# Performance work log

Hardware: AMD Instinct MI355X
Metric: run time of the kernel (lower is better)

## Reference

```python
import jax, jax.numpy as jnp
import numpy as np

BN_EPS = 1e-5


def setup_inputs() -> dict:
    key = jax.random.key(0)
    ks = jax.random.split(key, 12)
    N, F, H, E, ED, G, EMB = 59392, 116, 256, 950272, 5, 8, 16
    return {
        "x": jax.random.normal(ks[0], (N, F), dtype=jnp.float32),
        "edge_index": jax.random.randint(ks[1], (2, E), 0, N, dtype=jnp.int64),
        "edge_attr": jax.random.normal(ks[2], (E, ED), dtype=jnp.float32),
        "group_ids": jax.random.randint(ks[3], (N,), 0, G, dtype=jnp.int64),
        "group_emb": jax.random.normal(ks[4], (G, EMB), dtype=jnp.float32),
        "W_in": jax.random.normal(ks[5], (F + EMB, H), dtype=jnp.float32) * 0.05,
        "b_in": jnp.zeros((H,), dtype=jnp.float32),
        "gamma": jnp.ones((H,), dtype=jnp.float32),
        "beta": jnp.zeros((H,), dtype=jnp.float32),
        "We": jax.random.normal(ks[6], (ED, H), dtype=jnp.float32) * 0.05,
        "be": jnp.zeros((H,), dtype=jnp.float32),
        "W1": jax.random.normal(ks[7], (H, H), dtype=jnp.float32) * 0.05,
        "b1": jnp.zeros((H,), dtype=jnp.float32),
        "W2": jax.random.normal(ks[8], (H, H), dtype=jnp.float32) * 0.05,
        "b2": jnp.zeros((H,), dtype=jnp.float32),
    }


def reference(x, edge_index, edge_attr, group_ids, group_emb, W_in, b_in,
              gamma, beta, We, be, W1, b1, W2, b2):
    N = x.shape[0]
    # group-embedding concat (dropout is identity in eval mode)
    h = jnp.concatenate([x, group_emb[group_ids]], axis=-1)      # [N, F+EMB]
    # dynamically-created Linear + ReLU
    h = jax.nn.relu(h @ W_in + b_in)                              # [N, H]
    # BatchNorm over nodes (training stats, biased var)
    mu = jnp.mean(h, axis=0)
    var = jnp.mean(jnp.square(h - mu), axis=0)
    h = (h - mu) * jax.lax.rsqrt(var + BN_EPS) * gamma + beta
    # GINEConv: msg = ReLU(x_j + lin(edge_attr)); sum-aggregate at target
    src, dst = edge_index[0], edge_index[1]
    msg = jax.nn.relu(h[src] + edge_attr @ We + be)               # [E, H]
    agg = jax.ops.segment_sum(msg, dst, num_segments=N)          # [N, H]
    z = h + agg                                                   # (1+eps)*h, eps=0
    out = jax.nn.relu(z @ W1 + b1) @ W2 + b2                      # 2-layer MLP
    out = jax.nn.relu(out)
    return (out, edge_attr)
```

## Files before the change

kernel.cpp:

```cpp
#include <hip/hip_runtime.h>
#include <hip/hip_bf16.h>
#include <cstdint>
#include <cstddef>

#define H 256
#define EMB 16
#define ED 5
#define BN_EPS 1e-5f

typedef __attribute__((ext_vector_type(8))) short short8;
typedef __attribute__((ext_vector_type(4))) float f32x4;
typedef _Float16 h2 __attribute__((ext_vector_type(2)));

__device__ __forceinline__ unsigned short f2bf(float f) {
  unsigned int u = __float_as_uint(f);
  unsigned int r = (u + 0x7fffu + ((u >> 16) & 1u)) >> 16;
  return (unsigned short)r;
}
__device__ __forceinline__ unsigned int pk2bf(float a, float b) {
  return (unsigned int)f2bf(a) | ((unsigned int)f2bf(b) << 16);
}
__device__ __forceinline__ float bfhi(unsigned int u) {
  return __uint_as_float(u & 0xffff0000u);
}
__device__ __forceinline__ float bflo(unsigned int u) {
  return __uint_as_float(u << 16);
}
__device__ __forceinline__ h2 u2h2(unsigned int u) {
  union { unsigned int u; h2 h; } c;
  c.u = u;
  return c.h;
}
__device__ __forceinline__ unsigned int h22u(h2 h) {
  union { h2 h; unsigned int u; } c;
  c.h = h;
  return c.u;
}
__device__ __forceinline__ h2 mkh2(float a, float b) {
  h2 r;
  r.x = (_Float16)a;
  r.y = (_Float16)b;
  return r;
}

__global__ __launch_bounds__(256) void prep_kernel(
    const float* __restrict__ Win, const float* __restrict__ W1,
    const float* __restrict__ W2, const float* __restrict__ gemb,
    const float* __restrict__ b_in, unsigned short* __restrict__ Wtx,
    unsigned short* __restrict__ Wt1, unsigned short* __restrict__ Wt2,
    float* __restrict__ T, float* __restrict__ stats, int* __restrict__ deg,
    int N, int F, int G) {
  int idx = blockIdx.x * 256 + threadIdx.x;
  if (idx < 1024) stats[idx] = 0.f;
  if (idx < N) deg[idx] = 0;
  if (idx < 256 * 128) {
    int n = idx >> 7, k = idx & 127;
    Wtx[idx] = f2bf((k < F) ? Win[(size_t)k * H + n] : 0.f);
  } else if (idx < 256 * 128 + 65536) {
    int i2 = idx - 256 * 128;
    int n = i2 >> 8, k = i2 & 255;
    Wt1[i2] = f2bf(W1[(size_t)k * H + n]);
  } else if (idx < 256 * 128 + 131072) {
    int i2 = idx - 256 * 128 - 65536;
    int n = i2 >> 8, k = i2 & 255;
    Wt2[i2] = f2bf(W2[(size_t)k * H + n]);
  } else if (idx < 256 * 128 + 131072 + G * 256) {
    int i2 = idx - 256 * 128 - 131072;
    int g = i2 >> 8, c = i2 & 255;
    float s = b_in[c];
    #pragma unroll
    for (int k = 0; k < EMB; ++k)
      s = fmaf(gemb[g * EMB + k], Win[(size_t)(F + k) * H + c], s);
    T[i2] = s;
  }
}

__global__ __launch_bounds__(256) void gemm_in_kernel(
    const float* __restrict__ x, const int* __restrict__ gid,
    const unsigned short* __restrict__ Wtx, const float* __restrict__ T,
    unsigned short* __restrict__ h0, float* __restrict__ stats, int F) {
  const int m0 = blockIdx.y * 128;
  const int n0 = blockIdx.x * 128;
  const int tid = threadIdx.x;
  const int lane = tid & 63;
  const int wave = tid >> 6;
  const int wm = (wave & 1) * 64;
  const int wn = (wave >> 1) * 64;
  const int l16 = lane & 15;
  const int quad = lane >> 4;
  __shared__ __align__(16) unsigned short As[128][40];
  __shared__ __align__(16) unsigned short Bs[128][40];
  __shared__ float cs[128], css[128];
  if (tid < 128) {
    cs[tid] = 0.f;
    css[tid] = 0.f;
  }
  f32x4 acc[4][4] = {};
  const int srow = tid >> 1;
  const int half = tid & 1;
  for (int k0 = 0; k0 < 128; k0 += 32) {
    __syncthreads();
    {
      const float* xp = x + (size_t)(m0 + srow) * F;
      float4 xv[4];
      #pragma unroll
      for (int f = 0; f < 4; ++f) {
        int c = k0 + half * 16 + f * 4;
        xv[f] = (c < F) ? *(const float4*)(xp + c)
                        : make_float4(0.f, 0.f, 0.f, 0.f);
      }
      uint4 p0, p1;
      p0.x = pk2bf(xv[0].x, xv[0].y); p0.y = pk2bf(xv[0].z, xv[0].w);
      p0.z = pk2bf(xv[1].x, xv[1].y); p0.w = pk2bf(xv[1].z, xv[1].w);
      p1.x = pk2bf(xv[2].x, xv[2].y); p1.y = pk2bf(xv[2].z, xv[2].w);
      p1.z = pk2bf(xv[3].x, xv[3].y); p1.w = pk2bf(xv[3].z, xv[3].w);
      *(uint4*)(&As[srow][half * 16]) = p0;
      *(uint4*)(&As[srow][half * 16 + 8]) = p1;
    }
    {
      const unsigned short* wp = Wtx + (size_t)(n0 + srow) * 128 + k0 + half * 16;
      *(uint4*)(&Bs[srow][half * 16]) = *(const uint4*)wp;
      *(uint4*)(&Bs[srow][half * 16 + 8]) = *(const uint4*)(wp + 8);
    }
    __syncthreads();
    short8 af[4], bf[4];
    #pragma unroll
    for (int i = 0; i < 4; ++i)
      af[i] = *(const short8*)(&As[wm + i * 16 + l16][quad * 8]);
    #pragma unroll
    for (int j = 0; j < 4; ++j)
      bf[j] = *(const short8*)(&Bs[wn + j * 16 + l16][quad * 8]);
    #pragma unroll
    for (int i = 0; i < 4; ++i)
      #pragma unroll
      for (int j = 0; j < 4; ++j)
        acc[i][j] = __builtin_amdgcn_mfma_f32_16x16x32_bf16(af[i], bf[j],
                                                            acc[i][j], 0, 0, 0);
  }
  int gi[4][4];
  #pragma unroll
  for (int i = 0; i < 4; ++i)
    #pragma unroll
    for (int r = 0; r < 4; ++r)
      gi[i][r] = gid[m0 + wm + i * 16 + quad * 4 + r];
  float ls[4] = {}, lss[4] = {};
  #pragma unroll
  for (int j = 0; j < 4; ++j) {
    const int col = n0 + wn + j * 16 + l16;
    #pragma unroll
    for (int i = 0; i < 4; ++i) {
      #pragma unroll
      for (int r = 0; r < 4; ++r) {
        const int row = m0 + wm + i * 16 + quad * 4 + r;
        float v = fmaxf(acc[i][j][r] + T[gi[i][r] * H + col], 0.f);
        h0[(size_t)row * H + col] = f2bf(v);
        ls[j] += v;
        lss[j] = fmaf(v, v, lss[j]);
      }
    }
  }
  #pragma unroll
  for (int j = 0; j < 4; ++j) {
    const int lc = wn + j * 16 + l16;
    atomicAdd(&cs[lc], ls[j]);
    atomicAdd(&css[lc], lss[j]);
  }
  __syncthreads();
  if (tid < 128) {
    atomicAdd(&stats[n0 + tid], cs[tid]);
    atomicAdd(&stats[H + n0 + tid], css[tid]);
  }
}

__global__ __launch_bounds__(256) void mlp_kernel(
    const unsigned short* __restrict__ z, const unsigned short* __restrict__ Wt1,
    const unsigned short* __restrict__ Wt2, const float* __restrict__ b1,
    const float* __restrict__ b2, float* __restrict__ out) {
  const int m0 = blockIdx.x * 64;
  const int tid = threadIdx.x;
  const int lane = tid & 63;
  const int wave = tid >> 6;
  const int wn = wave * 64;
  const int l16 = lane & 15;
  const int quad = lane >> 4;
  __shared__ __align__(16) unsigned short As[64][40];
  __shared__ __align__(16) unsigned short Bs[256][40];
  __shared__ __align__(16) unsigned short hidS[64][264];
  f32x4 acc[4][4] = {};
  const int ar = tid >> 2, ac = tid & 3;
  for (int k0 = 0; k0 < 256; k0 += 32) {
    __syncthreads();
    *(float4*)(&As[ar][ac * 8]) =
        *(const float4*)(z + (size_t)(m0 + ar) * H + k0 + ac * 8);
    #pragma unroll
    for (int t = 0; t < 4; ++t) {
      int r = ar + t * 64;
      *(float4*)(&Bs[r][ac * 8]) =
          *(const float4*)(Wt1 + (size_t)r * H + k0 + ac * 8);
    }
    __syncthreads();
    short8 af[4], bf[4];
    #pragma unroll
    for (int i = 0; i < 4; ++i)
      af[i] = *(const short8*)(&As[i * 16 + l16][quad * 8]);
    #pragma unroll
    for (int j = 0; j < 4; ++j)
      bf[j] = *(const short8*)(&Bs[wn + j * 16 + l16][quad * 8]);
    #pragma unroll
    for (int i = 0; i < 4; ++i)
      #pragma unroll
      for (int j = 0; j < 4; ++j)
        acc[i][j] = __builtin_amdgcn_mfma_f32_16x16x32_bf16(af[i], bf[j],
                                                            acc[i][j], 0, 0, 0);
  }
  #pragma unroll
  for (int j = 0; j < 4; ++j) {
    const int col = wn + j * 16 + l16;
    const float bj = b1[col];
    #pragma unroll
    for (int i = 0; i < 4; ++i)
      #pragma unroll
      for (int r = 0; r < 4; ++r) {
        const int row = i * 16 + quad * 4 + r;
        hidS[row][col] = f2bf(fmaxf(acc[i][j][r] + bj, 0.f));
      }
  }
  #pragma unroll
  for (int i = 0; i < 4; ++i)
    #pragma unroll
    for (int j = 0; j < 4; ++j)
      acc[i][j] = (f32x4){0.f, 0.f, 0.f, 0.f};
  for (int k0 = 0; k0 < 256; k0 += 32) {
    __syncthreads();
    #pragma unroll
    for (int t = 0; t < 4; ++t) {
      int r = ar + t * 64;
      *(float4*)(&Bs[r][ac * 8]) =
          *(const float4*)(Wt2 + (size_t)r * H + k0 + ac * 8);
    }
    __syncthreads();
    short8 af[4], bf[4];
    #pragma unroll
    for (int i = 0; i < 4; ++i)
      af[i] = *(const short8*)(&hidS[i * 16 + l16][k0 + quad * 8]);
    #pragma unroll
    for (int j = 0; j < 4; ++j)
      bf[j] = *(const short8*)(&Bs[wn + j * 16 + l16][quad * 8]);
    #pragma unroll
    for (int i = 0; i < 4; ++i)
      #pragma unroll
      for (int j = 0; j < 4; ++j)
        acc[i][j] = __builtin_amdgcn_mfma_f32_16x16x32_bf16(af[i], bf[j],
                                                            acc[i][j], 0, 0, 0);
  }
  #pragma unroll
  for (int j = 0; j < 4; ++j) {
    const int col = wn + j * 16 + l16;
    const float bj = b2[col];
    #pragma unroll
    for (int i = 0; i < 4; ++i)
      #pragma unroll
      for (int r = 0; r < 4; ++r) {
        const int row = m0 + i * 16 + quad * 4 + r;
        out[(size_t)row * H + col] = fmaxf(acc[i][j][r] + bj, 0.f);
      }
  }
}

__global__ __launch_bounds__(256) void hbn_kernel(
    const unsigned short* __restrict__ h0, const float* __restrict__ stats,
    const float* __restrict__ gamma, const float* __restrict__ beta,
    const float* __restrict__ be, unsigned short* __restrict__ hbn,
    float inv_n) {
  __shared__ float sa[H], sb[H];
  {
    const int j = threadIdx.x;
    const float mu = stats[j] * inv_n;
    const float var = stats[H + j] * inv_n - mu * mu;
    const float rs = 1.0f / sqrtf(var + BN_EPS);
    const float a = gamma[j] * rs;
    sa[j] = a;
    sb[j] = beta[j] - mu * a + be[j];
  }
  __syncthreads();
  const size_t i = (size_t)blockIdx.x * 256 + threadIdx.x;
  const int c = ((int)(i & 31)) * 8;
  const uint4 hv = ((const uint4*)h0)[i];
  float r[8] = {bflo(hv.x), bfhi(hv.x), bflo(hv.y), bfhi(hv.y),
                bflo(hv.z), bfhi(hv.z), bflo(hv.w), bfhi(hv.w)};
  float o[8];
  #pragma unroll
  for (int t = 0; t < 8; ++t)
    o[t] = fmaf(sa[c + t], r[t], sb[c + t]);
  uint4 ov;
  ov.x = h22u(mkh2(o[0], o[1]));
  ov.y = h22u(mkh2(o[2], o[3]));
  ov.z = h22u(mkh2(o[4], o[5]));
  ov.w = h22u(mkh2(o[6], o[7]));
  ((uint4*)hbn)[i] = ov;
}

__global__ __launch_bounds__(256) void csr_count_kernel(
    const int* __restrict__ ei, int* __restrict__ deg, int E) {
  int e = blockIdx.x * 256 + threadIdx.x;
  if (e < E) atomicAdd(&deg[ei[E + e]], 1);
}

__global__ __launch_bounds__(256) void scan_blocks_kernel(
    const int* __restrict__ deg, int* __restrict__ excl,
    int* __restrict__ bsums, int n) {
  const int tid = threadIdx.x;
  const int i = blockIdx.x * 256 + tid;
  const int lane = tid & 63, wid = tid >> 6;
  int v = (i < n) ? deg[i] : 0;
  int x = v;
  #pragma unroll
  for (int d = 1; d < 64; d <<= 1) {
    int y = __shfl_up(x, d, 64);
    if (lane >= d) x += y;
  }
  __shared__ int ws[4], wo[4];
  if (lane == 63) ws[wid] = x;
  __syncthreads();
  if (tid == 0) {
    int a = 0;
    #pragma unroll
    for (int w = 0; w < 4; ++w) { wo[w] = a; a += ws[w]; }
    bsums[blockIdx.x] = a;
  }
  __syncthreads();
  if (i < n) excl[i] = x - v + wo[wid];
}

__global__ __launch_bounds__(256) void scan_finish_kernel(
    int* __restrict__ row_start, int* __restrict__ cursor,
    const int* __restrict__ bsums, int n, int E, int NB) {
  const int tid = threadIdx.x;
  const int b = blockIdx.x;
  int v = (tid < b && tid < NB) ? bsums[tid] : 0;
  int s = v;
  #pragma unroll
  for (int d = 32; d > 0; d >>= 1) s += __shfl_down(s, d, 64);
  __shared__ int ws[4];
  if ((tid & 63) == 0) ws[tid >> 6] = s;
  __syncthreads();
  const int S = ws[0] + ws[1] + ws[2] + ws[3];
  const int i = b * 256 + tid;
  if (i < n) {
    int r = row_start[i] + S;
    row_start[i] = r;
    cursor[i] = r;
  }
  if (b == 0 && tid == 0) row_start[n] = E;
}

__global__ __launch_bounds__(256) void csr_scatter_kernel(
    const int* __restrict__ ei, const float* __restrict__ ea,
    int* __restrict__ cursor, uint4* __restrict__ rec,
    float* __restrict__ ea_out, int E) {
  int e = blockIdx.x * 256 + threadIdx.x;
  if (e >= E) return;
  int s = ei[e];
  int d = ei[E + e];
  int p = atomicAdd(&cursor[d], 1);
  const float* eap = ea + (size_t)e * ED;
  const float e0 = eap[0], e1 = eap[1], e2 = eap[2], e3 = eap[3], e4 = eap[4];
  uint4 r;
  r.x = (unsigned)s;
  r.y = h22u(mkh2(e0, e1));
  r.z = h22u(mkh2(e2, e3));
  r.w = h22u(mkh2(e4, 0.f));
  rec[p] = r;
  float* op = ea_out + (size_t)e * ED;
  op[0] = e0; op[1] = e1; op[2] = e2; op[3] = e3; op[4] = e4;
}

__device__ __forceinline__ void edge_accum(
    const uint4 rr, const uint2 hv, const h2 wA[5], const h2 wB[5],
    float& ax, float& ay, float& az, float& aw) {
  h2 m01 = u2h2(hv.x);
  h2 m23 = u2h2(hv.y);
  const h2 e01 = u2h2(rr.y), e23 = u2h2(rr.z), e44 = u2h2(rr.w);
  h2 t;
  t.x = e01.x; t.y = e01.x;  m01 += t * wA[0]; m23 += t * wB[0];
  t.x = e01.y; t.y = e01.y;  m01 += t * wA[1]; m23 += t * wB[1];
  t.x = e23.x; t.y = e23.x;  m01 += t * wA[2]; m23 += t * wB[2];
  t.x = e23.y; t.y = e23.y;  m01 += t * wA[3]; m23 += t * wB[3];
  t.x = e44.x; t.y = e44.x;  m01 += t * wA[4]; m23 += t * wB[4];
  const h2 z2 = {(_Float16)0.f, (_Float16)0.f};
  m01 = __builtin_elementwise_max(m01, z2);
  m23 = __builtin_elementwise_max(m23, z2);
  ax += (float)m01.x;
  ay += (float)m01.y;
  az += (float)m23.x;
  aw += (float)m23.y;
}

__global__ __launch_bounds__(256) void aggregate_kernel(
    const unsigned short* __restrict__ hbn, const uint4* __restrict__ rec,
    const float* __restrict__ We, const float* __restrict__ be,
    const int* __restrict__ row_start, unsigned short* __restrict__ z,
    int N) {
  const int lane = threadIdx.x & 63;
  int n = blockIdx.x * 4 + (threadIdx.x >> 6);
  if (n >= N) return;
  n = __builtin_amdgcn_readfirstlane(n);
  const int c = lane * 4;
  const float4 be4 = *(const float4*)(be + c);
  h2 wA[5], wB[5];
  #pragma unroll
  for (int k = 0; k < 5; ++k) {
    wA[k] = mkh2(We[k * H + c], We[k * H + c + 1]);
    wB[k] = mkh2(We[k * H + c + 2], We[k * H + c + 3]);
  }
  float ax = 0.f, ay = 0.f, az = 0.f, aw = 0.f;
  const int s0 = __builtin_amdgcn_readfirstlane(row_start[n]);
  const int s1 = __builtin_amdgcn_readfirstlane(row_start[n + 1]);
  const uint4* rp = rec + s0;
  const int cnt = s1 - s0;
  int i = 0;
  for (; i + 8 <= cnt; i += 8) {
    uint4 rr[8];
    uint2 hh[8];
    #pragma unroll
    for (int u = 0; u < 8; ++u) rr[u] = rp[i + u];
    #pragma unroll
    for (int u = 0; u < 8; ++u)
      hh[u] = *(const uint2*)(hbn + (size_t)(int)rr[u].x * H + c);
    #pragma unroll
    for (int u = 0; u < 8; ++u)
      edge_accum(rr[u], hh[u], wA, wB, ax, ay, az, aw);
  }
  for (; i + 4 <= cnt; i += 4) {
    uint4 rr[4];
    uint2 hh[4];
    #pragma unroll
    for (int u = 0; u < 4; ++u) rr[u] = rp[i + u];
    #pragma unroll
    for (int u = 0; u < 4; ++u)
      hh[u] = *(const uint2*)(hbn + (size_t)(int)rr[u].x * H + c);
    #pragma unroll
    for (int u = 0; u < 4; ++u)
      edge_accum(rr[u], hh[u], wA, wB, ax, ay, az, aw);
  }
  for (; i < cnt; ++i) {
    const uint4 r0 = rp[i];
    const uint2 h0v = *(const uint2*)(hbn + (size_t)(int)r0.x * H + c);
    edge_accum(r0, h0v, wA, wB, ax, ay, az, aw);
  }
  const uint2 hs = *(const uint2*)(hbn + (size_t)n * H + c);
  const h2 hsA = u2h2(hs.x), hsB = u2h2(hs.y);
  float zx = (float)hsA.x - be4.x + ax;
  float zy = (float)hsA.y - be4.y + ay;
  float zz = (float)hsB.x - be4.z + az;
  float zw = (float)hsB.y - be4.w + aw;
  uint2 o;
  o.x = pk2bf(zx, zy);
  o.y = pk2bf(zz, zw);
  *(uint2*)(z + (size_t)n * H + c) = o;
}

extern "C" void kernel_launch(void* const* d_in, const int* in_sizes, int n_in,
                              void* d_out, int out_size, void* d_ws, size_t ws_size,
                              hipStream_t stream) {
  const float* x     = (const float*)d_in[0];
  const int*   ei    = (const int*)d_in[1];
  const float* ea    = (const float*)d_in[2];
  const int*   gid   = (const int*)d_in[3];
  const float* gemb  = (const float*)d_in[4];
  const float* W_in  = (const float*)d_in[5];
  const float* b_in  = (const float*)d_in[6];
  const float* gamma = (const float*)d_in[7];
  const float* beta  = (const float*)d_in[8];
  const float* We    = (const float*)d_in[9];
  const float* be    = (const float*)d_in[10];
  const float* W1    = (const float*)d_in[11];
  const float* b1    = (const float*)d_in[12];
  const float* W2    = (const float*)d_in[13];
  const float* b2    = (const float*)d_in[14];
  float* out = (float*)d_out;

  const int N = in_sizes[3];
  const int E = in_sizes[1] / 2;
  const int F = in_sizes[0] / N;
  const int G = in_sizes[4] / EMB;
  const int NB = (N + 255) / 256;

  char* p = (char*)d_ws;
  auto take = [&](size_t bytes) {
    char* r = p;
    p += (bytes + 255) & ~(size_t)255;
    return r;
  };
  float* stats          = (float*)take(1024 * sizeof(float));
  int* deg              = (int*)take((size_t)N * 4);
  int* row_start        = (int*)take((size_t)(N + 1) * 4);
  int* cursor           = (int*)take((size_t)N * 4);
  int* bsums            = (int*)take((size_t)NB * 4);
  uint4* rec            = (uint4*)take((size_t)E * 16);
  unsigned short* Wtx   = (unsigned short*)take((size_t)256 * 128 * 2);
  unsigned short* Wt1   = (unsigned short*)take((size_t)H * H * 2);
  unsigned short* Wt2   = (unsigned short*)take((size_t)H * H * 2);
  float* T              = (float*)take((size_t)G * H * 4);
  unsigned short* h0    = (unsigned short*)take((size_t)N * H * 2);
  unsigned short* hbn   = (unsigned short*)take((size_t)N * H * 2);
  unsigned short* z     = (unsigned short*)take((size_t)N * H * 2);

  {
    int total = 256 * 128 + 131072 + G * 256;
    int nb = (total + 255) / 256;
    if (nb < (N + 255) / 256) nb = (N + 255) / 256;
    prep_kernel<<<nb, 256, 0, stream>>>(W_in, W1, W2, gemb, b_in, Wtx, Wt1,
                                        Wt2, T, stats, deg, N, F, G);
  }

  csr_count_kernel<<<(E + 255) / 256, 256, 0, stream>>>(ei, deg, E);
  scan_blocks_kernel<<<NB, 256, 0, stream>>>(deg, row_start, bsums, N);
  scan_finish_kernel<<<NB, 256, 0, stream>>>(row_start, cursor, bsums, N, E, NB);
  csr_scatter_kernel<<<(E + 255) / 256, 256, 0, stream>>>(
      ei, ea, cursor, rec, out + (size_t)N * H, E);

  dim3 ggrid(H / 128, N / 128);
  gemm_in_kernel<<<ggrid, 256, 0, stream>>>(x, gid, Wtx, T, h0, stats, F);

  hbn_kernel<<<((size_t)N * H / 8) / 256, 256, 0, stream>>>(
      h0, stats, gamma, beta, be, hbn, 1.0f / (float)N);

  aggregate_kernel<<<(N + 3) / 4, 256, 0, stream>>>(hbn, rec, We, be,
                                                    row_start, z, N);

  mlp_kernel<<<N / 64, 256, 0, stream>>>(z, Wt1, Wt2, b1, b2, out);
}
```

Before: 391.0 us.

## Fuse aggregation into MLP and merge independent CSR and prep launches

Edge aggregation now runs inside the MLP kernel. Each block aggregates 64 nodes straight into shared memory, then runs both GEMMs on them, so the z buffer is never written to or read back from global memory. The degree count is merged into the prep kernel and the CSR scatter into the input GEMM kernel as separate block ranges, and zeroing moves to a hipMemsetAsync, which cuts the number of launches. The cost is lower parallelism during aggregation: one wave handles 16 nodes serially with an unroll of 4 instead of 8, and the ~59k-node aggregation is spread over only N/64 blocks.

```diff
diff --git a/kernel.cpp b/kernel.cpp
--- a/kernel.cpp
+++ b/kernel.cpp
@@ -43,16 +43,19 @@
   return r;
 }
 
-__global__ __launch_bounds__(256) void prep_kernel(
+__global__ __launch_bounds__(256) void count_prep_kernel(
+    const int* __restrict__ ei, int* __restrict__ deg,
     const float* __restrict__ Win, const float* __restrict__ W1,
     const float* __restrict__ W2, const float* __restrict__ gemb,
     const float* __restrict__ b_in, unsigned short* __restrict__ Wtx,
     unsigned short* __restrict__ Wt1, unsigned short* __restrict__ Wt2,
-    float* __restrict__ T, float* __restrict__ stats, int* __restrict__ deg,
-    int N, int F, int G) {
-  int idx = blockIdx.x * 256 + threadIdx.x;
-  if (idx < 1024) stats[idx] = 0.f;
-  if (idx < N) deg[idx] = 0;
+    float* __restrict__ T, int E, int F, int G, int CB) {
+  if ((int)blockIdx.x < CB) {
+    int e = blockIdx.x * 256 + threadIdx.x;
+    if (e < E) atomicAdd(&deg[ei[E + e]], 1);
+    return;
+  }
+  int idx = (blockIdx.x - CB) * 256 + threadIdx.x;
   if (idx < 256 * 128) {
     int n = idx >> 7, k = idx & 127;
     Wtx[idx] = f2bf((k < F) ? Win[(size_t)k * H + n] : 0.f);
@@ -75,12 +78,86 @@
   }
 }
 
-__global__ __launch_bounds__(256) void gemm_in_kernel(
+__global__ __launch_bounds__(256) void scan_blocks_kernel(
+    const int* __restrict__ deg, int* __restrict__ excl,
+    int* __restrict__ bsums, int n) {
+  const int tid = threadIdx.x;
+  const int i = blockIdx.x * 256 + tid;
+  const int lane = tid & 63, wid = tid >> 6;
+  int v = (i < n) ? deg[i] : 0;
+  int x = v;
+  #pragma unroll
+  for (int d = 1; d < 64; d <<= 1) {
+    int y = __shfl_up(x, d, 64);
+    if (lane >= d) x += y;
+  }
+  __shared__ int ws[4], wo[4];
+  if (lane == 63) ws[wid] = x;
+  __syncthreads();
+  if (tid == 0) {
+    int a = 0;
+    #pragma unroll
+    for (int w = 0; w < 4; ++w) { wo[w] = a; a += ws[w]; }
+    bsums[blockIdx.x] = a;
+  }
+  __syncthreads();
+  if (i < n) excl[i] = x - v + wo[wid];
+}
+
+__global__ __launch_bounds__(256) void scan_finish_kernel(
+    int* __restrict__ row_start, int* __restrict__ cursor,
+    const int* __restrict__ bsums, int n, int E, int NB) {
+  const int tid = threadIdx.x;
+  const int b = blockIdx.x;
+  int v = (tid < b && tid < NB) ? bsums[tid] : 0;
+  int s = v;
+  #pragma unroll
+  for (int d = 32; d > 0; d >>= 1) s += __shfl_down(s, d, 64);
+  __shared__ int ws[4];
+  if ((tid & 63) == 0) ws[tid >> 6] = s;
+  __syncthreads();
+  const int S = ws[0] + ws[1] + ws[2] + ws[3];
+  const int i = b * 256 + tid;
+  if (i < n) {
+    int r = row_start[i] + S;
+    row_start[i] = r;
+    cursor[i] = r;
+  }
+  if (b == 0 && tid == 0) row_start[n] = E;
+}
+
+__global__ __launch_bounds__(256) void scatter_gemm_kernel(
+    const int* __restrict__ ei, const float* __restrict__ ea,
+    int* __restrict__ cursor, uint4* __restrict__ rec,
+    float* __restrict__ ea_out,
     const float* __restrict__ x, const int* __restrict__ gid,
     const unsigned short* __restrict__ Wtx, const float* __restrict__ T,
-    unsigned short* __restrict__ h0, float* __restrict__ stats, int F) {
-  const int m0 = blockIdx.y * 128;
-  const int n0 = blockIdx.x * 128;
+    unsigned short* __restrict__ h0, float* __restrict__ stats,
+    int E, int F, int SB) {
+  __shared__ __align__(16) unsigned short As[128][40];
+  __shared__ __align__(16) unsigned short Bs[128][40];
+  __shared__ float cs[128], css[128];
+  if ((int)blockIdx.x < SB) {
+    int e = blockIdx.x * 256 + threadIdx.x;
+    if (e >= E) return;
+    int s = ei[e];
+    int d = ei[E + e];
+    int p = atomicAdd(&cursor[d], 1);
+    const float* eap = ea + (size_t)e * ED;
+    const float e0 = eap[0], e1 = eap[1], e2 = eap[2], e3 = eap[3], e4 = eap[4];
+    uint4 r;
+    r.x = (unsigned)s;
+    r.y = h22u(mkh2(e0, e1));
+    r.z = h22u(mkh2(e2, e3));
+    r.w = h22u(mkh2(e4, 0.f));
+    rec[p] = r;
+    float* op = ea_out + (size_t)e * ED;
+    op[0] = e0; op[1] = e1; op[2] = e2; op[3] = e3; op[4] = e4;
+    return;
+  }
+  const int bx = blockIdx.x - SB;
+  const int m0 = (bx >> 1) * 128;
+  const int n0 = (bx & 1) * 128;
   const int tid = threadIdx.x;
   const int lane = tid & 63;
   const int wave = tid >> 6;
@@ -88,9 +165,6 @@
   const int wn = (wave >> 1) * 64;
   const int l16 = lane & 15;
   const int quad = lane >> 4;
-  __shared__ __align__(16) unsigned short As[128][40];
-  __shared__ __align__(16) unsigned short Bs[128][40];
-  __shared__ float cs[128], css[128];
   if (tid < 128) {
     cs[tid] = 0.f;
     css[tid] = 0.f;
@@ -169,101 +243,6 @@
   if (tid < 128) {
     atomicAdd(&stats[n0 + tid], cs[tid]);
     atomicAdd(&stats[H + n0 + tid], css[tid]);
-  }
-}
-
-__global__ __launch_bounds__(256) void mlp_kernel(
-    const unsigned short* __restrict__ z, const unsigned short* __restrict__ Wt1,
-    const unsigned short* __restrict__ Wt2, const float* __restrict__ b1,
-    const float* __restrict__ b2, float* __restrict__ out) {
-  const int m0 = blockIdx.x * 64;
-  const int tid = threadIdx.x;
-  const int lane = tid & 63;
-  const int wave = tid >> 6;
-  const int wn = wave * 64;
-  const int l16 = lane & 15;
-  const int quad = lane >> 4;
-  __shared__ __align__(16) unsigned short As[64][40];
-  __shared__ __align__(16) unsigned short Bs[256][40];
-  __shared__ __align__(16) unsigned short hidS[64][264];
-  f32x4 acc[4][4] = {};
-  const int ar = tid >> 2, ac = tid & 3;
-  for (int k0 = 0; k0 < 256; k0 += 32) {
-    __syncthreads();
-    *(float4*)(&As[ar][ac * 8]) =
-        *(const float4*)(z + (size_t)(m0 + ar) * H + k0 + ac * 8);
-    #pragma unroll
-    for (int t = 0; t < 4; ++t) {
-      int r = ar + t * 64;
-      *(float4*)(&Bs[r][ac * 8]) =
-          *(const float4*)(Wt1 + (size_t)r * H + k0 + ac * 8);
-    }
-    __syncthreads();
-    short8 af[4], bf[4];
-    #pragma unroll
-    for (int i = 0; i < 4; ++i)
-      af[i] = *(const short8*)(&As[i * 16 + l16][quad * 8]);
-    #pragma unroll
-    for (int j = 0; j < 4; ++j)
-      bf[j] = *(const short8*)(&Bs[wn + j * 16 + l16][quad * 8]);
-    #pragma unroll
-    for (int i = 0; i < 4; ++i)
-      #pragma unroll
-      for (int j = 0; j < 4; ++j)
-        acc[i][j] = __builtin_amdgcn_mfma_f32_16x16x32_bf16(af[i], bf[j],
-                                                            acc[i][j], 0, 0, 0);
-  }
-  #pragma unroll
-  for (int j = 0; j < 4; ++j) {
-    const int col = wn + j * 16 + l16;
-    const float bj = b1[col];
-    #pragma unroll
-    for (int i = 0; i < 4; ++i)
-      #pragma unroll
-      for (int r = 0; r < 4; ++r) {
-        const int row = i * 16 + quad * 4 + r;
-        hidS[row][col] = f2bf(fmaxf(acc[i][j][r] + bj, 0.f));
-      }
-  }
-  #pragma unroll
-  for (int i = 0; i < 4; ++i)
-    #pragma unroll
-    for (int j = 0; j < 4; ++j)
-      acc[i][j] = (f32x4){0.f, 0.f, 0.f, 0.f};
-  for (int k0 = 0; k0 < 256; k0 += 32) {
-    __syncthreads();
-    #pragma unroll
-    for (int t = 0; t < 4; ++t) {
-      int r = ar + t * 64;
-      *(float4*)(&Bs[r][ac * 8]) =
-          *(const float4*)(Wt2 + (size_t)r * H + k0 + ac * 8);
-    }
-    __syncthreads();
-    short8 af[4], bf[4];
-    #pragma unroll
-    for (int i = 0; i < 4; ++i)
-      af[i] = *(const short8*)(&hidS[i * 16 + l16][k0 + quad * 8]);
-    #pragma unroll
-    for (int j = 0; j < 4; ++j)
-      bf[j] = *(const short8*)(&Bs[wn + j * 16 + l16][quad * 8]);
-    #pragma unroll
-    for (int i = 0; i < 4; ++i)
-      #pragma unroll
-      for (int j = 0; j < 4; ++j)
-        acc[i][j] = __builtin_amdgcn_mfma_f32_16x16x32_bf16(af[i], bf[j],
-                                                            acc[i][j], 0, 0, 0);
-  }
-  #pragma unroll
-  for (int j = 0; j < 4; ++j) {
-    const int col = wn + j * 16 + l16;
-    const float bj = b2[col];
-    #pragma unroll
-    for (int i = 0; i < 4; ++i)
-      #pragma unroll
-      for (int r = 0; r < 4; ++r) {
-        const int row = m0 + i * 16 + quad * 4 + r;
-        out[(size_t)row * H + col] = fmaxf(acc[i][j][r] + bj, 0.f);
-      }
   }
 }
 
@@ -298,81 +277,6 @@
   ov.z = h22u(mkh2(o[4], o[5]));
   ov.w = h22u(mkh2(o[6], o[7]));
   ((uint4*)hbn)[i] = ov;
-}
-
-__global__ __launch_bounds__(256) void csr_count_kernel(
-    const int* __restrict__ ei, int* __restrict__ deg, int E) {
-  int e = blockIdx.x * 256 + threadIdx.x;
-  if (e < E) atomicAdd(&deg[ei[E + e]], 1);
-}
-
-__global__ __launch_bounds__(256) void scan_blocks_kernel(
-    const int* __restrict__ deg, int* __restrict__ excl,
-    int* __restrict__ bsums, int n) {
-  const int tid = threadIdx.x;
-  const int i = blockIdx.x * 256 + tid;
-  const int lane = tid & 63, wid = tid >> 6;
-  int v = (i < n) ? deg[i] : 0;
-  int x = v;
-  #pragma unroll
-  for (int d = 1; d < 64; d <<= 1) {
-    int y = __shfl_up(x, d, 64);
-    if (lane >= d) x += y;
-  }
-  __shared__ int ws[4], wo[4];
-  if (lane == 63) ws[wid] = x;
-  __syncthreads();
-  if (tid == 0) {
-    int a = 0;
-    #pragma unroll
-    for (int w = 0; w < 4; ++w) { wo[w] = a; a += ws[w]; }
-    bsums[blockIdx.x] = a;
-  }
-  __syncthreads();
-  if (i < n) excl[i] = x - v + wo[wid];
-}
-
-__global__ __launch_bounds__(256) void scan_finish_kernel(
-    int* __restrict__ row_start, int* __restrict__ cursor,
-    const int* __restrict__ bsums, int n, int E, int NB) {
-  const int tid = threadIdx.x;
-  const int b = blockIdx.x;
-  int v = (tid < b && tid < NB) ? bsums[tid] : 0;
-  int s = v;
-  #pragma unroll
-  for (int d = 32; d > 0; d >>= 1) s += __shfl_down(s, d, 64);
-  __shared__ int ws[4];
-  if ((tid & 63) == 0) ws[tid >> 6] = s;
-  __syncthreads();
-  const int S = ws[0] + ws[1] + ws[2] + ws[3];
-  const int i = b * 256 + tid;
-  if (i < n) {
-    int r = row_start[i] + S;
-    row_start[i] = r;
-    cursor[i] = r;
-  }
-  if (b == 0 && tid == 0) row_start[n] = E;
-}
-
-__global__ __launch_bounds__(256) void csr_scatter_kernel(
-    const int* __restrict__ ei, const float* __restrict__ ea,
-    int* __restrict__ cursor, uint4* __restrict__ rec,
-    float* __restrict__ ea_out, int E) {
-  int e = blockIdx.x * 256 + threadIdx.x;
-  if (e >= E) return;
-  int s = ei[e];
-  int d = ei[E + e];
-  int p = atomicAdd(&cursor[d], 1);
-  const float* eap = ea + (size_t)e * ED;
-  const float e0 = eap[0], e1 = eap[1], e2 = eap[2], e3 = eap[3], e4 = eap[4];
-  uint4 r;
-  r.x = (unsigned)s;
-  r.y = h22u(mkh2(e0, e1));
-  r.z = h22u(mkh2(e2, e3));
-  r.w = h22u(mkh2(e4, 0.f));
-  rec[p] = r;
-  float* op = ea_out + (size_t)e * ED;
-  op[0] = e0; op[1] = e1; op[2] = e2; op[3] = e3; op[4] = e4;
 }
 
 __device__ __forceinline__ void edge_accum(
@@ -396,68 +300,144 @@
   aw += (float)m23.y;
 }
 
-__global__ __launch_bounds__(256) void aggregate_kernel(
+__global__ __launch_bounds__(256) void agg_mlp_kernel(
     const unsigned short* __restrict__ hbn, const uint4* __restrict__ rec,
     const float* __restrict__ We, const float* __restrict__ be,
-    const int* __restrict__ row_start, unsigned short* __restrict__ z,
-    int N) {
-  const int lane = threadIdx.x & 63;
-  int n = blockIdx.x * 4 + (threadIdx.x >> 6);
-  if (n >= N) return;
-  n = __builtin_amdgcn_readfirstlane(n);
-  const int c = lane * 4;
-  const float4 be4 = *(const float4*)(be + c);
-  h2 wA[5], wB[5];
-  #pragma unroll
-  for (int k = 0; k < 5; ++k) {
-    wA[k] = mkh2(We[k * H + c], We[k * H + c + 1]);
-    wB[k] = mkh2(We[k * H + c + 2], We[k * H + c + 3]);
-  }
-  float ax = 0.f, ay = 0.f, az = 0.f, aw = 0.f;
-  const int s0 = __builtin_amdgcn_readfirstlane(row_start[n]);
-  const int s1 = __builtin_amdgcn_readfirstlane(row_start[n + 1]);
-  const uint4* rp = rec + s0;
-  const int cnt = s1 - s0;
-  int i = 0;
-  for (; i + 8 <= cnt; i += 8) {
-    uint4 rr[8];
-    uint2 hh[8];
-    #pragma unroll
-    for (int u = 0; u < 8; ++u) rr[u] = rp[i + u];
-    #pragma unroll
-    for (int u = 0; u < 8; ++u)
-      hh[u] = *(const uint2*)(hbn + (size_t)(int)rr[u].x * H + c);
-    #pragma unroll
-    for (int u = 0; u < 8; ++u)
-      edge_accum(rr[u], hh[u], wA, wB, ax, ay, az, aw);
-  }
-  for (; i + 4 <= cnt; i += 4) {
-    uint4 rr[4];
-    uint2 hh[4];
-    #pragma unroll
-    for (int u = 0; u < 4; ++u) rr[u] = rp[i + u];
-    #pragma unroll
-    for (int u = 0; u < 4; ++u)
-      hh[u] = *(const uint2*)(hbn + (size_t)(int)rr[u].x * H + c);
-    #pragma unroll
-    for (int u = 0; u < 4; ++u)
-      edge_accum(rr[u], hh[u], wA, wB, ax, ay, az, aw);
-  }
-  for (; i < cnt; ++i) {
-    const uint4 r0 = rp[i];
-    const uint2 h0v = *(const uint2*)(hbn + (size_t)(int)r0.x * H + c);
-    edge_accum(r0, h0v, wA, wB, ax, ay, az, aw);
-  }
-  const uint2 hs = *(const uint2*)(hbn + (size_t)n * H + c);
-  const h2 hsA = u2h2(hs.x), hsB = u2h2(hs.y);
-  float zx = (float)hsA.x - be4.x + ax;
-  float zy = (float)hsA.y - be4.y + ay;
-  float zz = (float)hsB.x - be4.z + az;
-  float zw = (float)hsB.y - be4.w + aw;
-  uint2 o;
-  o.x = pk2bf(zx, zy);
-  o.y = pk2bf(zz, zw);
-  *(uint2*)(z + (size_t)n * H + c) = o;
+    const int* __restrict__ row_start,
+    const unsigned short* __restrict__ Wt1,
+    const unsigned short* __restrict__ Wt2, const float* __restrict__ b1,
+    const float* __restrict__ b2, float* __restrict__ out, int N) {
+  const int tid = threadIdx.x;
+  const int lane = tid & 63;
+  const int wave = tid >> 6;
+  const int m0 = blockIdx.x * 64;
+  __shared__ __align__(16) unsigned short zS[64][264];
+  __shared__ __align__(16) unsigned short Bs[256][40];
+  {
+    const int c = lane * 4;
+    const float4 be4 = *(const float4*)(be + c);
+    h2 wA[5], wB[5];
+    #pragma unroll
+    for (int k = 0; k < 5; ++k) {
+      wA[k] = mkh2(We[k * H + c], We[k * H + c + 1]);
+      wB[k] = mkh2(We[k * H + c + 2], We[k * H + c + 3]);
+    }
+    for (int t = 0; t < 16; ++t) {
+      const int n = __builtin_amdgcn_readfirstlane(m0 + wave * 16 + t);
+      const int s0 = __builtin_amdgcn_readfirstlane(row_start[n]);
+      const int s1 = __builtin_amdgcn_readfirstlane(row_start[n + 1]);
+      const uint4* rp = rec + s0;
+      const int cnt = s1 - s0;
+      float ax = 0.f, ay = 0.f, az = 0.f, aw = 0.f;
+      int i = 0;
+      for (; i + 4 <= cnt; i += 4) {
+        uint4 rr[4];
+        uint2 hh[4];
+        #pragma unroll
+        for (int u = 0; u < 4; ++u) rr[u] = rp[i + u];
+        #pragma unroll
+        for (int u = 0; u < 4; ++u)
+          hh[u] = *(const uint2*)(hbn + (size_t)(int)rr[u].x * H + c);
+        #pragma unroll
+        for (int u = 0; u < 4; ++u)
+          edge_accum(rr[u], hh[u], wA, wB, ax, ay, az, aw);
+      }
+      for (; i < cnt; ++i) {
+        const uint4 r0 = rp[i];
+        const uint2 h0v = *(const uint2*)(hbn + (size_t)(int)r0.x * H + c);
+        edge_accum(r0, h0v, wA, wB, ax, ay, az, aw);
+      }
+      const uint2 hs = *(const uint2*)(hbn + (size_t)n * H + c);
+      const h2 hsA = u2h2(hs.x), hsB = u2h2(hs.y);
+      uint2 o;
+      o.x = pk2bf((float)hsA.x - be4.x + ax, (float)hsA.y - be4.y + ay);
+      o.y = pk2bf((float)hsB.x - be4.z + az, (float)hsB.y - be4.w + aw);
+      *(uint2*)(&zS[wave * 16 + t][c]) = o;
+    }
+  }
+  __syncthreads();
+  const int l16 = lane & 15;
+  const int quad = lane >> 4;
+  const int wn = wave * 64;
+  const int ar = tid >> 2, ac = tid & 3;
+  f32x4 acc[4][4] = {};
+  for (int k0 = 0; k0 < 256; k0 += 32) {
+    __syncthreads();
+    #pragma unroll
+    for (int t = 0; t < 4; ++t) {
+      int r = ar + t * 64;
+      *(float4*)(&Bs[r][ac * 8]) =
+          *(const float4*)(Wt1 + (size_t)r * H + k0 + ac * 8);
+    }
+    __syncthreads();
+    short8 af[4], bf[4];
+    #pragma unroll
+    for (int i = 0; i < 4; ++i)
+      af[i] = *(const short8*)(&zS[i * 16 + l16][k0 + quad * 8]);
+    #pragma unroll
+    for (int j = 0; j < 4; ++j)
+      bf[j] = *(const short8*)(&Bs[wn + j * 16 + l16][quad * 8]);
+    #pragma unroll
+    for (int i = 0; i < 4; ++i)
+      #pragma unroll
+      for (int j = 0; j < 4; ++j)
+        acc[i][j] = __builtin_amdgcn_mfma_f32_16x16x32_bf16(af[i], bf[j],
+                                                            acc[i][j], 0, 0, 0);
+  }
+  __syncthreads();
+  #pragma unroll
+  for (int j = 0; j < 4; ++j) {
+    const int col = wn + j * 16 + l16;
+    const float bj = b1[col];
+    #pragma unroll
+    for (int i = 0; i < 4; ++i)
+      #pragma unroll
+      for (int r = 0; r < 4; ++r) {
+        const int row = i * 16 + quad * 4 + r;
+        zS[row][col] = f2bf(fmaxf(acc[i][j][r] + bj, 0.f));
+      }
+  }
+  #pragma unroll
+  for (int i = 0; i < 4; ++i)
+    #pragma unroll
+    for (int j = 0; j < 4; ++j)
+      acc[i][j] = (f32x4){0.f, 0.f, 0.f, 0.f};
+  __syncthreads();
+  for (int k0 = 0; k0 < 256; k0 += 32) {
+    __syncthreads();
+    #pragma unroll
+    for (int t = 0; t < 4; ++t) {
+      int r = ar + t * 64;
+      *(float4*)(&Bs[r][ac * 8]) =
+          *(const float4*)(Wt2 + (size_t)r * H + k0 + ac * 8);
+    }
+    __syncthreads();
+    short8 af[4], bf[4];
+    #pragma unroll
+    for (int i = 0; i < 4; ++i)
+      af[i] = *(const short8*)(&zS[i * 16 + l16][k0 + quad * 8]);
+    #pragma unroll
+    for (int j = 0; j < 4; ++j)
+      bf[j] = *(const short8*)(&Bs[wn + j * 16 + l16][quad * 8]);
+    #pragma unroll
+    for (int i = 0; i < 4; ++i)
+      #pragma unroll
+      for (int j = 0; j < 4; ++j)
+        acc[i][j] = __builtin_amdgcn_mfma_f32_16x16x32_bf16(af[i], bf[j],
+                                                            acc[i][j], 0, 0, 0);
+  }
+  #pragma unroll
+  for (int j = 0; j < 4; ++j) {
+    const int col = wn + j * 16 + l16;
+    const float bj = b2[col];
+    #pragma unroll
+    for (int i = 0; i < 4; ++i)
+      #pragma unroll
+      for (int r = 0; r < 4; ++r) {
+        const int row = m0 + i * 16 + quad * 4 + r;
+        out[(size_t)row * H + col] = fmaxf(acc[i][j][r] + bj, 0.f);
+      }
+  }
 }
 
 extern "C" void kernel_launch(void* const* d_in, const int* in_sizes, int n_in,
@@ -485,6 +465,7 @@
   const int F = in_sizes[0] / N;
   const int G = in_sizes[4] / EMB;
   const int NB = (N + 255) / 256;
+  const int CB = (E + 255) / 256;
 
   char* p = (char*)d_ws;
   auto take = [&](size_t bytes) {
@@ -492,7 +473,7 @@
     p += (bytes + 255) & ~(size_t)255;
     return r;
   };
-  float* stats          = (float*)take(1024 * sizeof(float));
+  float* stats          = (float*)take(4096);
   int* deg              = (int*)take((size_t)N * 4);
   int* row_start        = (int*)take((size_t)(N + 1) * 4);
   int* cursor           = (int*)take((size_t)N * 4);
@@ -504,30 +485,27 @@
   float* T              = (float*)take((size_t)G * H * 4);
   unsigned short* h0    = (unsigned short*)take((size_t)N * H * 2);
   unsigned short* hbn   = (unsigned short*)take((size_t)N * H * 2);
-  unsigned short* z     = (unsigned short*)take((size_t)N * H * 2);
+
+  (void)hipMemsetAsync(stats, 0, 4096 + (size_t)N * 4, stream);
 
   {
-    int total = 256 * 128 + 131072 + G * 256;
-    int nb = (total + 255) / 256;
-    if (nb < (N + 255) / 256) nb = (N + 255) / 256;
-    prep_kernel<<<nb, 256, 0, stream>>>(W_in, W1, W2, gemb, b_in, Wtx, Wt1,
-                                        Wt2, T, stats, deg, N, F, G);
-  }
-
-  csr_count_kernel<<<(E + 255) / 256, 256, 0, stream>>>(ei, deg, E);
+    int prep_total = 256 * 128 + 131072 + G * 256;
+    int nb = CB + (prep_total + 255) / 256;
+    count_prep_kernel<<<nb, 256, 0, stream>>>(ei, deg, W_in, W1, W2, gemb,
+                                              b_in, Wtx, Wt1, Wt2, T, E, F, G,
+                                              CB);
+  }
+
   scan_blocks_kernel<<<NB, 256, 0, stream>>>(deg, row_start, bsums, N);
   scan_finish_kernel<<<NB, 256, 0, stream>>>(row_start, cursor, bsums, N, E, NB);
-  csr_scatter_kernel<<<(E + 255) / 256, 256, 0, stream>>>(
-      ei, ea, cursor, rec, out + (size_t)N * H, E);
-
-  dim3 ggrid(H / 128, N / 128);
-  gemm_in_kernel<<<ggrid, 256, 0, stream>>>(x, gid, Wtx, T, h0, stats, F);
+
+  scatter_gemm_kernel<<<CB + (N / 128) * 2, 256, 0, stream>>>(
+      ei, ea, cursor, rec, out + (size_t)N * H, x, gid, Wtx, T, h0, stats, E,
+      F, CB);
 
   hbn_kernel<<<((size_t)N * H / 8) / 256, 256, 0, stream>>>(
       h0, stats, gamma, beta, be, hbn, 1.0f / (float)N);
 
-  aggregate_kernel<<<(N + 3) / 4, 256, 0, stream>>>(hbn, rec, We, be,
-                                                    row_start, z, N);
-
-  mlp_kernel<<<N / 64, 256, 0, stream>>>(z, Wt1, Wt2, b1, b2, out);
-}
+  agg_mlp_kernel<<<N / 64, 256, 0, stream>>>(hbn, rec, We, be, row_start, Wt1,
+                                             Wt2, b1, b2, out, N);
+}
```

Result: slower. 451.6 us (+15.5%).
